# Kernel tuning notes

Measured on AMD Instinct MI355X. Metric: run time of the kernel, lower is better.

Reference implementation:

```python
import jax, jax.numpy as jnp
import numpy as np

H = 16        # num_attention_heads
D = 1024      # hidden_size
HD = D // H   # head_dim = 64


def setup_inputs() -> dict:
    key = jax.random.key(0)
    ks = jax.random.split(key, 5)
    B, T = 16, 1024
    s_in = 1.0 / np.sqrt(D)
    return {
        "hidden_states": jax.random.normal(ks[0], (B, T, D), dtype=jnp.float32),
        "w_qkv": jax.random.normal(ks[1], (D, 3 * D), dtype=jnp.float32) * s_in,
        "b_qkv": jnp.zeros((3 * D,), dtype=jnp.float32),
        "w_out": jax.random.normal(ks[2], (D, D), dtype=jnp.float32) * s_in,
        "b_out": jnp.zeros((D,), dtype=jnp.float32),
    }


def reference(hidden_states, w_qkv, b_qkv, w_out, b_out):
    B, T, C = hidden_states.shape
    qkv = hidden_states @ w_qkv + b_qkv                      # [B,T,3C]
    q, k, v = jnp.split(qkv, 3, axis=-1)
    # [B,T,C] -> [B,H,T,HD]
    q = q.reshape(B, T, H, HD).transpose(0, 2, 1, 3)
    k = k.reshape(B, T, H, HD).transpose(0, 2, 1, 3)
    v = v.reshape(B, T, H, HD).transpose(0, 2, 1, 3)
    scale = 1.0 / np.sqrt(HD)
    logits = jnp.einsum("bhqd,bhkd->bhqk", q, k) * scale     # [B,H,T,T]
    attn = jax.nn.softmax(logits, axis=-1)
    out = jnp.einsum("bhqk,bhkd->bhqd", attn, v)             # [B,H,T,HD]
    out = out.transpose(0, 2, 1, 3).reshape(B, T, C)
    return out @ w_out + b_out
```

## Files before the change

kernel.cpp:

```cpp
#include <hip/hip_runtime.h>
#include <cstdint>
#include <cstddef>

typedef _Float16 h8 __attribute__((ext_vector_type(8)));
typedef _Float16 h4 __attribute__((ext_vector_type(4)));
typedef float f4 __attribute__((ext_vector_type(4)));

#define MFMA(a, b, c) __builtin_amdgcn_mfma_f32_16x16x32_f16((a), (b), (c), 0, 0, 0)

__device__ __forceinline__ void gl_lds16(const void* g, void* l) {
  __builtin_amdgcn_global_load_lds((const __attribute__((address_space(1))) void*)g,
                                   (__attribute__((address_space(3))) void*)l, 16, 0, 0);
}

__global__ void k_cvt_hs(const float* __restrict__ in, _Float16* __restrict__ out, int n8) {
  int i = blockIdx.x * blockDim.x + threadIdx.x;
  if (i >= n8) return;
  size_t idx = (size_t)i * 8;
  float4 a = *(const float4*)(in + idx);
  float4 b = *(const float4*)(in + idx + 4);
  h8 o;
  o[0] = (_Float16)a.x; o[1] = (_Float16)a.y; o[2] = (_Float16)a.z; o[3] = (_Float16)a.w;
  o[4] = (_Float16)b.x; o[5] = (_Float16)b.y; o[6] = (_Float16)b.z; o[7] = (_Float16)b.w;
  *(h8*)(out + idx) = o;
}

__global__ void k_transcvt(const float* __restrict__ in, _Float16* __restrict__ out, int N, int K) {
  __shared__ float tile[64 * 65];
  int tn = blockIdx.x * 64, tk = blockIdx.y * 64;
  for (int i = 0; i < 4; ++i) {
    int cid = i * 256 + threadIdx.x;
    int r = cid >> 4, c4 = cid & 15;
    float4 v = *(const float4*)(in + (size_t)(tk + r) * N + tn + c4 * 4);
    tile[r * 65 + c4 * 4 + 0] = v.x; tile[r * 65 + c4 * 4 + 1] = v.y;
    tile[r * 65 + c4 * 4 + 2] = v.z; tile[r * 65 + c4 * 4 + 3] = v.w;
  }
  __syncthreads();
  for (int i = 0; i < 2; ++i) {
    int cid = i * 256 + threadIdx.x;
    int n = cid >> 3, kc = cid & 7;
    h8 o;
    for (int j = 0; j < 8; ++j) o[j] = (_Float16)tile[(kc * 8 + j) * 65 + n];
    *(h8*)(out + (size_t)(tn + n) * K + tk + kc * 8) = o;
  }
}

__global__ void k_transpose_v(const _Float16* __restrict__ V, _Float16* __restrict__ Vt) {
  __shared__ _Float16 tile[64 * 66];
  int bh = blockIdx.x;
  int tt = blockIdx.y * 64;
  const _Float16* src = V + (size_t)bh * 65536 + (size_t)tt * 64;
  _Float16* dst = Vt + (size_t)bh * 65536 + tt;
  for (int i = 0; i < 2; ++i) {
    int cid = i * 256 + threadIdx.x;
    int r = cid >> 3, c8 = cid & 7;
    h8 v = *(const h8*)(src + (size_t)r * 64 + c8 * 8);
    for (int j = 0; j < 8; ++j) tile[r * 66 + c8 * 8 + j] = v[j];
  }
  __syncthreads();
  for (int i = 0; i < 2; ++i) {
    int cid = i * 256 + threadIdx.x;
    int d = cid >> 3, tc = cid & 7;
    h8 o;
    for (int j = 0; j < 8; ++j) o[j] = tile[(tc * 8 + j) * 66 + d];
    *(h8*)(dst + (size_t)d * 1024 + tc * 8) = o;
  }
}

__global__ __launch_bounds__(256) void k_gemm_qkv(
    const _Float16* __restrict__ A, const _Float16* __restrict__ BT,
    const float* __restrict__ bias,
    _Float16* __restrict__ Q, _Float16* __restrict__ Kq, _Float16* __restrict__ V) {
  __shared__ _Float16 sA[128 * 64];
  __shared__ _Float16 sB[128 * 64];
  const int K = 1024;
  int tid = threadIdx.x, wave = tid >> 6, lane = tid & 63;
  int l15 = lane & 15, l4 = lane >> 4;
  int tm = blockIdx.y * 128, tn = blockIdx.x * 128;
  int wm = (wave & 1) * 64, wn = (wave >> 1) * 64;
  f4 acc[4][4] = {};
  for (int kt = 0; kt < K; kt += 64) {
    __syncthreads();
    for (int i = 0; i < 4; ++i) {
      int cid = i * 256 + tid;
      int r = cid >> 3, cs = cid & 7, cg = cs ^ (r & 7);
      gl_lds16(A + (size_t)(tm + r) * K + kt + cg * 8, (char*)sA + cid * 16);
      gl_lds16(BT + (size_t)(tn + r) * K + kt + cg * 8, (char*)sB + cid * 16);
    }
    __syncthreads();
    for (int k0 = 0; k0 < 64; k0 += 32) {
      h8 af[4], bf[4];
      int ch = (k0 >> 3) + l4;
      for (int mi = 0; mi < 4; ++mi) {
        int r = wm + mi * 16 + l15;
        af[mi] = *(const h8*)((const char*)sA + ((r * 8 + (ch ^ (r & 7))) * 16));
      }
      for (int ni = 0; ni < 4; ++ni) {
        int r = wn + ni * 16 + l15;
        bf[ni] = *(const h8*)((const char*)sB + ((r * 8 + (ch ^ (r & 7))) * 16));
      }
      for (int mi = 0; mi < 4; ++mi)
        for (int ni = 0; ni < 4; ++ni)
          acc[mi][ni] = MFMA(af[mi], bf[ni], acc[mi][ni]);
    }
  }
  for (int mi = 0; mi < 4; ++mi) {
    for (int ni = 0; ni < 4; ++ni) {
      int n = tn + wn + ni * 16 + l15;
      float bv = bias[n];
      int which = n >> 10, h = (n >> 6) & 15, d = n & 63;
      _Float16* dst = which == 0 ? Q : (which == 1 ? Kq : V);
      for (int r = 0; r < 4; ++r) {
        int m = tm + wm + mi * 16 + l4 * 4 + r;
        int b = m >> 10, t = m & 1023;
        dst[(((size_t)b * 16 + h) * 1024 + t) * 64 + d] = (_Float16)(acc[mi][ni][r] + bv);
      }
    }
  }
}

__global__ __launch_bounds__(256, 4) void k_attn(
    const _Float16* __restrict__ Q, const _Float16* __restrict__ Kk,
    const _Float16* __restrict__ Vt, _Float16* __restrict__ O) {
  __shared__ char smem[18432 + 8192 + 8192];
  _Float16* sQ = (_Float16*)smem;
  _Float16* sP = (_Float16*)smem;
  _Float16* sK = (_Float16*)(smem + 18432);
  _Float16* sV = (_Float16*)(smem + 18432 + 8192);
  const float SCL = 0.125f * 1.44269504088896340736f;
  int tid = threadIdx.x, wave = tid >> 6, lane = tid & 63;
  int l15 = lane & 15, l4 = lane >> 4;
  int bh = blockIdx.y;
  int qt = blockIdx.x * 128;
  const _Float16* Qb = Q + (size_t)bh * 65536;
  const _Float16* Kb = Kk + (size_t)bh * 65536;
  const _Float16* Vb = Vt + (size_t)bh * 65536;

  for (int i = 0; i < 4; ++i) {
    int cid = i * 256 + tid;
    int r = cid >> 3, cs = cid & 7, cg = cs ^ (r & 7);
    gl_lds16(Qb + (size_t)(qt + r) * 64 + cg * 8, (char*)sQ + cid * 16);
  }
  __syncthreads();
  h8 qf[2][2];
  for (int nt = 0; nt < 2; ++nt) {
    int r = wave * 32 + nt * 16 + l15;
    for (int kk = 0; kk < 2; ++kk) {
      int ch = kk * 4 + l4;
      qf[nt][kk] = *(const h8*)((const char*)sQ + ((r * 8 + (ch ^ (r & 7))) * 16));
    }
  }
  _Float16 scl_h = (_Float16)SCL;
  for (int nt = 0; nt < 2; ++nt)
    for (int kk = 0; kk < 2; ++kk)
      for (int j = 0; j < 8; ++j) qf[nt][kk][j] *= scl_h;

  float lpart[2] = {0.f, 0.f};
  f4 oacc[2][4] = {};
  _Float16* pw = sP + wave * 32 * 72;

  for (int kt = 0; kt < 1024; kt += 64) {
    __syncthreads();
    for (int i = 0; i < 2; ++i) {
      int cid = i * 256 + tid;
      int r = cid >> 3, cs = cid & 7, cg = cs ^ (r & 7);
      gl_lds16(Kb + (size_t)(kt + r) * 64 + cg * 8, (char*)sK + cid * 16);
      gl_lds16(Vb + (size_t)r * 1024 + kt + cg * 8, (char*)sV + cid * 16);
    }
    __syncthreads();
    f4 sacc[4][2] = {};
    for (int kk = 0; kk < 2; ++kk) {
      h8 kf[4];
      int ch = kk * 4 + l4;
      for (int mt = 0; mt < 4; ++mt) {
        int r = mt * 16 + l15;
        kf[mt] = *(const h8*)((const char*)sK + ((r * 8 + (ch ^ (r & 7))) * 16));
      }
      for (int mt = 0; mt < 4; ++mt)
        for (int nt = 0; nt < 2; ++nt)
          sacc[mt][nt] = MFMA(kf[mt], qf[nt][kk], sacc[mt][nt]);
    }
    for (int mt = 0; mt < 4; ++mt) {
      for (int nt = 0; nt < 2; ++nt) {
        float p0 = exp2f(sacc[mt][nt][0]);
        float p1 = exp2f(sacc[mt][nt][1]);
        float p2 = exp2f(sacc[mt][nt][2]);
        float p3 = exp2f(sacc[mt][nt][3]);
        lpart[nt] += (p0 + p1) + (p2 + p3);
        h4 pk;
        pk[0] = (_Float16)p0; pk[1] = (_Float16)p1;
        pk[2] = (_Float16)p2; pk[3] = (_Float16)p3;
        *(h4*)(pw + (nt * 16 + l15) * 72 + mt * 16 + l4 * 4) = pk;
      }
    }
    for (int kk = 0; kk < 2; ++kk) {
      h8 pf[2], vf[4];
      for (int mi = 0; mi < 2; ++mi)
        pf[mi] = *(const h8*)(pw + (mi * 16 + l15) * 72 + kk * 32 + l4 * 8);
      int ch = kk * 4 + l4;
      for (int nd = 0; nd < 4; ++nd) {
        int r = nd * 16 + l15;
        vf[nd] = *(const h8*)((const char*)sV + ((r * 8 + (ch ^ (r & 7))) * 16));
      }
      for (int mi = 0; mi < 2; ++mi)
        for (int nd = 0; nd < 4; ++nd)
          oacc[mi][nd] = MFMA(pf[mi], vf[nd], oacc[mi][nd]);
    }
  }
  float lt[2];
  lt[0] = lpart[0]; lt[1] = lpart[1];
  for (int nt = 0; nt < 2; ++nt) {
    lt[nt] += __shfl_xor(lt[nt], 16);
    lt[nt] += __shfl_xor(lt[nt], 32);
  }
  int b = bh >> 4, h = bh & 15;
  for (int mi = 0; mi < 2; ++mi) {
    for (int r = 0; r < 4; ++r) {
      float lr = __shfl(lt[mi], l4 * 4 + r);
      float inv = 1.f / lr;
      int t = qt + wave * 32 + mi * 16 + l4 * 4 + r;
      for (int nd = 0; nd < 4; ++nd)
        O[(size_t)(b * 1024 + t) * 1024 + h * 64 + nd * 16 + l15] =
            (_Float16)(oacc[mi][nd][r] * inv);
    }
  }
}

__global__ __launch_bounds__(256) void k_gemm_out(
    const _Float16* __restrict__ A, const _Float16* __restrict__ BT,
    const float* __restrict__ bias, float* __restrict__ C) {
  __shared__ _Float16 sA[128 * 64];
  __shared__ _Float16 sB[128 * 64];
  const int K = 1024;
  int tid = threadIdx.x, wave = tid >> 6, lane = tid & 63;
  int l15 = lane & 15, l4 = lane >> 4;
  int tm = blockIdx.y * 128, tn = blockIdx.x * 128;
  int wm = (wave & 1) * 64, wn = (wave >> 1) * 64;
  f4 acc[4][4] = {};
  for (int kt = 0; kt < K; kt += 64) {
    __syncthreads();
    for (int i = 0; i < 4; ++i) {
      int cid = i * 256 + tid;
      int r = cid >> 3, cs = cid & 7, cg = cs ^ (r & 7);
      gl_lds16(A + (size_t)(tm + r) * K + kt + cg * 8, (char*)sA + cid * 16);
      gl_lds16(BT + (size_t)(tn + r) * K + kt + cg * 8, (char*)sB + cid * 16);
    }
    __syncthreads();
    for (int k0 = 0; k0 < 64; k0 += 32) {
      h8 af[4], bf[4];
      int ch = (k0 >> 3) + l4;
      for (int mi = 0; mi < 4; ++mi) {
        int r = wm + mi * 16 + l15;
        af[mi] = *(const h8*)((const char*)sA + ((r * 8 + (ch ^ (r & 7))) * 16));
      }
      for (int ni = 0; ni < 4; ++ni) {
        int r = wn + ni * 16 + l15;
        bf[ni] = *(const h8*)((const char*)sB + ((r * 8 + (ch ^ (r & 7))) * 16));
      }
      for (int mi = 0; mi < 4; ++mi)
        for (int ni = 0; ni < 4; ++ni)
          acc[mi][ni] = MFMA(af[mi], bf[ni], acc[mi][ni]);
    }
  }
  for (int mi = 0; mi < 4; ++mi) {
    for (int ni = 0; ni < 4; ++ni) {
      int n = tn + wn + ni * 16 + l15;
      float bv = bias[n];
      for (int r = 0; r < 4; ++r) {
        int m = tm + wm + mi * 16 + l4 * 4 + r;
        C[(size_t)m * 1024 + n] = acc[mi][ni][r] + bv;
      }
    }
  }
}

extern "C" void kernel_launch(void* const* d_in, const int* in_sizes, int n_in,
                              void* d_out, int out_size, void* d_ws, size_t ws_size,
                              hipStream_t stream) {
  const float* hs    = (const float*)d_in[0];
  const float* w_qkv = (const float*)d_in[1];
  const float* b_qkv = (const float*)d_in[2];
  const float* w_out = (const float*)d_in[3];
  const float* b_out = (const float*)d_in[4];
  float* out = (float*)d_out;
  char* ws = (char*)d_ws;

  _Float16* hs_h  = (_Float16*)(ws);
  _Float16* wqkvT = (_Float16*)(ws + 33554432);
  _Float16* woutT = (_Float16*)(ws + 39845888);
  _Float16* q_ws  = (_Float16*)(ws + 41943040);
  _Float16* k_ws  = (_Float16*)(ws + 75497472);
  _Float16* v_ws  = (_Float16*)(ws + 109051904);
  _Float16* vt_ws = (_Float16*)(ws + 142606336);

  k_cvt_hs<<<8192, 256, 0, stream>>>(hs, hs_h, 2097152);
  k_transcvt<<<dim3(48, 16), 256, 0, stream>>>(w_qkv, wqkvT, 3072, 1024);
  k_transcvt<<<dim3(16, 16), 256, 0, stream>>>(w_out, woutT, 1024, 1024);
  k_gemm_qkv<<<dim3(24, 128), 256, 0, stream>>>(hs_h, wqkvT, b_qkv, q_ws, k_ws, v_ws);
  k_transpose_v<<<dim3(256, 16), 256, 0, stream>>>(v_ws, vt_ws);
  _Float16* attn_h = hs_h;
  k_attn<<<dim3(8, 256), 256, 0, stream>>>(q_ws, k_ws, vt_ws, attn_h);
  k_gemm_out<<<dim3(8, 128), 256, 0, stream>>>(attn_h, woutT, b_out, out);
}
```

Measured before the change: 435.7 us.

## Fuse V transpose into QKV GEMM epilogue and enlarge attention query tile

The QKV GEMM epilogue now writes V directly in transposed [b,h,d,t] layout by staging the tile in shared memory, which removes the separate transpose kernel and its extra pass over V in global memory. The attention kernel now processes 256 queries per block (64 per wave) instead of 128, so each K/V tile loaded into LDS is reused across twice as many queries. In exchange the attention kernel uses more registers and LDS, and launch bounds drop to 3 blocks per CU, which lowers occupancy.

```diff
diff --git a/kernel.cpp b/kernel.cpp
--- a/kernel.cpp
+++ b/kernel.cpp
@@ -45,34 +45,13 @@
   }
 }
 
-__global__ void k_transpose_v(const _Float16* __restrict__ V, _Float16* __restrict__ Vt) {
-  __shared__ _Float16 tile[64 * 66];
-  int bh = blockIdx.x;
-  int tt = blockIdx.y * 64;
-  const _Float16* src = V + (size_t)bh * 65536 + (size_t)tt * 64;
-  _Float16* dst = Vt + (size_t)bh * 65536 + tt;
-  for (int i = 0; i < 2; ++i) {
-    int cid = i * 256 + threadIdx.x;
-    int r = cid >> 3, c8 = cid & 7;
-    h8 v = *(const h8*)(src + (size_t)r * 64 + c8 * 8);
-    for (int j = 0; j < 8; ++j) tile[r * 66 + c8 * 8 + j] = v[j];
-  }
-  __syncthreads();
-  for (int i = 0; i < 2; ++i) {
-    int cid = i * 256 + threadIdx.x;
-    int d = cid >> 3, tc = cid & 7;
-    h8 o;
-    for (int j = 0; j < 8; ++j) o[j] = tile[(tc * 8 + j) * 66 + d];
-    *(h8*)(dst + (size_t)d * 1024 + tc * 8) = o;
-  }
-}
-
 __global__ __launch_bounds__(256) void k_gemm_qkv(
     const _Float16* __restrict__ A, const _Float16* __restrict__ BT,
     const float* __restrict__ bias,
-    _Float16* __restrict__ Q, _Float16* __restrict__ Kq, _Float16* __restrict__ V) {
-  __shared__ _Float16 sA[128 * 64];
-  __shared__ _Float16 sB[128 * 64];
+    _Float16* __restrict__ Q, _Float16* __restrict__ Kq, _Float16* __restrict__ Vt) {
+  __shared__ char smem[32768];
+  _Float16* sA = (_Float16*)smem;
+  _Float16* sB = (_Float16*)(smem + 16384);
   const int K = 1024;
   int tid = threadIdx.x, wave = tid >> 6, lane = tid & 63;
   int l15 = lane & 15, l4 = lane >> 4;
@@ -104,60 +83,91 @@
           acc[mi][ni] = MFMA(af[mi], bf[ni], acc[mi][ni]);
     }
   }
-  for (int mi = 0; mi < 4; ++mi) {
-    for (int ni = 0; ni < 4; ++ni) {
-      int n = tn + wn + ni * 16 + l15;
-      float bv = bias[n];
-      int which = n >> 10, h = (n >> 6) & 15, d = n & 63;
-      _Float16* dst = which == 0 ? Q : (which == 1 ? Kq : V);
-      for (int r = 0; r < 4; ++r) {
-        int m = tm + wm + mi * 16 + l4 * 4 + r;
-        int b = m >> 10, t = m & 1023;
-        dst[(((size_t)b * 16 + h) * 1024 + t) * 64 + d] = (_Float16)(acc[mi][ni][r] + bv);
-      }
-    }
-  }
-}
-
-__global__ __launch_bounds__(256, 4) void k_attn(
+  if (blockIdx.x < 16) {
+    for (int mi = 0; mi < 4; ++mi) {
+      for (int ni = 0; ni < 4; ++ni) {
+        int n = tn + wn + ni * 16 + l15;
+        float bv = bias[n];
+        int which = n >> 10, h = (n >> 6) & 15, d = n & 63;
+        _Float16* dst = which == 0 ? Q : Kq;
+        for (int r = 0; r < 4; ++r) {
+          int m = tm + wm + mi * 16 + l4 * 4 + r;
+          int b = m >> 10, t = m & 1023;
+          dst[(((size_t)b * 16 + h) * 1024 + t) * 64 + d] = (_Float16)(acc[mi][ni][r] + bv);
+        }
+      }
+    }
+  } else {
+    _Float16* L = (_Float16*)smem;
+    int b = tm >> 10, tbase = tm & 1023;
+    for (int pass = 0; pass < 2; ++pass) {
+      __syncthreads();
+      if ((wave & 1) == pass) {
+        for (int mi = 0; mi < 4; ++mi) {
+          int t_local = mi * 16 + l4 * 4;
+          for (int ni = 0; ni < 4; ++ni) {
+            int n_local = wn + ni * 16 + l15;
+            float bv = bias[tn + n_local];
+            h4 pk;
+            for (int r = 0; r < 4; ++r) pk[r] = (_Float16)(acc[mi][ni][r] + bv);
+            *(h4*)(L + n_local * 68 + t_local) = pk;
+          }
+        }
+      }
+      __syncthreads();
+      for (int it = 0; it < 2; ++it) {
+        int n_local = it * 64 + (tid >> 2);
+        int h = (tn - 2048 + n_local) >> 6;
+        int d = n_local & 63;
+        size_t row = (((size_t)b * 16 + h) * 64 + d) * 1024 + tbase + pass * 64;
+        for (int j = 0; j < 2; ++j) {
+          int th = (tid & 3) * 8 + j * 32;
+          *(h8*)(Vt + row + th) = *(const h8*)(L + n_local * 68 + th);
+        }
+      }
+    }
+  }
+}
+
+__global__ __launch_bounds__(256, 3) void k_attn(
     const _Float16* __restrict__ Q, const _Float16* __restrict__ Kk,
     const _Float16* __restrict__ Vt, _Float16* __restrict__ O) {
-  __shared__ char smem[18432 + 8192 + 8192];
+  __shared__ char smem[36864 + 8192 + 8192];
   _Float16* sQ = (_Float16*)smem;
   _Float16* sP = (_Float16*)smem;
-  _Float16* sK = (_Float16*)(smem + 18432);
-  _Float16* sV = (_Float16*)(smem + 18432 + 8192);
+  _Float16* sK = (_Float16*)(smem + 36864);
+  _Float16* sV = (_Float16*)(smem + 36864 + 8192);
   const float SCL = 0.125f * 1.44269504088896340736f;
   int tid = threadIdx.x, wave = tid >> 6, lane = tid & 63;
   int l15 = lane & 15, l4 = lane >> 4;
   int bh = blockIdx.y;
-  int qt = blockIdx.x * 128;
+  int qt = blockIdx.x * 256;
   const _Float16* Qb = Q + (size_t)bh * 65536;
   const _Float16* Kb = Kk + (size_t)bh * 65536;
   const _Float16* Vb = Vt + (size_t)bh * 65536;
 
-  for (int i = 0; i < 4; ++i) {
+  for (int i = 0; i < 8; ++i) {
     int cid = i * 256 + tid;
     int r = cid >> 3, cs = cid & 7, cg = cs ^ (r & 7);
     gl_lds16(Qb + (size_t)(qt + r) * 64 + cg * 8, (char*)sQ + cid * 16);
   }
   __syncthreads();
-  h8 qf[2][2];
-  for (int nt = 0; nt < 2; ++nt) {
-    int r = wave * 32 + nt * 16 + l15;
+  h8 qf[4][2];
+  for (int nt = 0; nt < 4; ++nt) {
+    int r = wave * 64 + nt * 16 + l15;
     for (int kk = 0; kk < 2; ++kk) {
       int ch = kk * 4 + l4;
       qf[nt][kk] = *(const h8*)((const char*)sQ + ((r * 8 + (ch ^ (r & 7))) * 16));
     }
   }
   _Float16 scl_h = (_Float16)SCL;
-  for (int nt = 0; nt < 2; ++nt)
+  for (int nt = 0; nt < 4; ++nt)
     for (int kk = 0; kk < 2; ++kk)
       for (int j = 0; j < 8; ++j) qf[nt][kk][j] *= scl_h;
 
-  float lpart[2] = {0.f, 0.f};
-  f4 oacc[2][4] = {};
-  _Float16* pw = sP + wave * 32 * 72;
+  float lpart[4] = {0.f, 0.f, 0.f, 0.f};
+  f4 oacc[4][4] = {};
+  _Float16* pw = sP + wave * 64 * 72;
 
   for (int kt = 0; kt < 1024; kt += 64) {
     __syncthreads();
@@ -168,57 +178,59 @@
       gl_lds16(Vb + (size_t)r * 1024 + kt + cg * 8, (char*)sV + cid * 16);
     }
     __syncthreads();
-    f4 sacc[4][2] = {};
+    for (int mh = 0; mh < 2; ++mh) {
+      f4 sacc[2][4] = {};
+      for (int kk = 0; kk < 2; ++kk) {
+        h8 kf[2];
+        int ch = kk * 4 + l4;
+        for (int mt = 0; mt < 2; ++mt) {
+          int r = mh * 32 + mt * 16 + l15;
+          kf[mt] = *(const h8*)((const char*)sK + ((r * 8 + (ch ^ (r & 7))) * 16));
+        }
+        for (int mt = 0; mt < 2; ++mt)
+          for (int nt = 0; nt < 4; ++nt)
+            sacc[mt][nt] = MFMA(kf[mt], qf[nt][kk], sacc[mt][nt]);
+      }
+      for (int mt = 0; mt < 2; ++mt) {
+        for (int nt = 0; nt < 4; ++nt) {
+          float p0 = exp2f(sacc[mt][nt][0]);
+          float p1 = exp2f(sacc[mt][nt][1]);
+          float p2 = exp2f(sacc[mt][nt][2]);
+          float p3 = exp2f(sacc[mt][nt][3]);
+          lpart[nt] += (p0 + p1) + (p2 + p3);
+          h4 pk;
+          pk[0] = (_Float16)p0; pk[1] = (_Float16)p1;
+          pk[2] = (_Float16)p2; pk[3] = (_Float16)p3;
+          *(h4*)(pw + (nt * 16 + l15) * 72 + mh * 32 + mt * 16 + l4 * 4) = pk;
+        }
+      }
+    }
     for (int kk = 0; kk < 2; ++kk) {
-      h8 kf[4];
-      int ch = kk * 4 + l4;
-      for (int mt = 0; mt < 4; ++mt) {
-        int r = mt * 16 + l15;
-        kf[mt] = *(const h8*)((const char*)sK + ((r * 8 + (ch ^ (r & 7))) * 16));
-      }
-      for (int mt = 0; mt < 4; ++mt)
-        for (int nt = 0; nt < 2; ++nt)
-          sacc[mt][nt] = MFMA(kf[mt], qf[nt][kk], sacc[mt][nt]);
-    }
-    for (int mt = 0; mt < 4; ++mt) {
-      for (int nt = 0; nt < 2; ++nt) {
-        float p0 = exp2f(sacc[mt][nt][0]);
-        float p1 = exp2f(sacc[mt][nt][1]);
-        float p2 = exp2f(sacc[mt][nt][2]);
-        float p3 = exp2f(sacc[mt][nt][3]);
-        lpart[nt] += (p0 + p1) + (p2 + p3);
-        h4 pk;
-        pk[0] = (_Float16)p0; pk[1] = (_Float16)p1;
-        pk[2] = (_Float16)p2; pk[3] = (_Float16)p3;
-        *(h4*)(pw + (nt * 16 + l15) * 72 + mt * 16 + l4 * 4) = pk;
-      }
-    }
-    for (int kk = 0; kk < 2; ++kk) {
-      h8 pf[2], vf[4];
-      for (int mi = 0; mi < 2; ++mi)
+      h8 pf[4], vf[4];
+      for (int mi = 0; mi < 4; ++mi)
         pf[mi] = *(const h8*)(pw + (mi * 16 + l15) * 72 + kk * 32 + l4 * 8);
       int ch = kk * 4 + l4;
       for (int nd = 0; nd < 4; ++nd) {
         int r = nd * 16 + l15;
         vf[nd] = *(const h8*)((const char*)sV + ((r * 8 + (ch ^ (r & 7))) * 16));
       }
-      for (int mi = 0; mi < 2; ++mi)
+      for (int mi = 0; mi < 4; ++mi)
         for (int nd = 0; nd < 4; ++nd)
           oacc[mi][nd] = MFMA(pf[mi], vf[nd], oacc[mi][nd]);
     }
   }
-  float lt[2];
-  lt[0] = lpart[0]; lt[1] = lpart[1];
-  for (int nt = 0; nt < 2; ++nt) {
+  float lt[4];
+  for (int nt = 0; nt < 4; ++nt) {
+    lt[nt] = lpart[nt];
     lt[nt] += __shfl_xor(lt[nt], 16);
     lt[nt] += __shfl_xor(lt[nt], 32);
   }
   int b = bh >> 4, h = bh & 15;
-  for (int mi = 0; mi < 2; ++mi) {
+  for (int mi = 0; mi < 4; ++mi) {
     for (int r = 0; r < 4; ++r) {
       float lr = __shfl(lt[mi], l4 * 4 + r);
       float inv = 1.f / lr;
-      int t = qt + wave * 32 + mi * 16 + l4 * 4 + r;
+      int t = qt + wave * 64 + mi * 16 + l4 * 4 + r;
       for (int nd = 0; nd < 4; ++nd)
         O[(size_t)(b * 1024 + t) * 1024 + h * 64 + nd * 16 + l15] =
             (_Float16)(oacc[mi][nd][r] * inv);
@@ -290,15 +302,13 @@
   _Float16* woutT = (_Float16*)(ws + 39845888);
   _Float16* q_ws  = (_Float16*)(ws + 41943040);
   _Float16* k_ws  = (_Float16*)(ws + 75497472);
-  _Float16* v_ws  = (_Float16*)(ws + 109051904);
-  _Float16* vt_ws = (_Float16*)(ws + 142606336);
+  _Float16* vt_ws = (_Float16*)(ws + 109051904);
 
   k_cvt_hs<<<8192, 256, 0, stream>>>(hs, hs_h, 2097152);
   k_transcvt<<<dim3(48, 16), 256, 0, stream>>>(w_qkv, wqkvT, 3072, 1024);
   k_transcvt<<<dim3(16, 16), 256, 0, stream>>>(w_out, woutT, 1024, 1024);
-  k_gemm_qkv<<<dim3(24, 128), 256, 0, stream>>>(hs_h, wqkvT, b_qkv, q_ws, k_ws, v_ws);
-  k_transpose_v<<<dim3(256, 16), 256, 0, stream>>>(v_ws, vt_ws);
+  k_gemm_qkv<<<dim3(24, 128), 256, 0, stream>>>(hs_h, wqkvT, b_qkv, q_ws, k_ws, vt_ws);
   _Float16* attn_h = hs_h;
-  k_attn<<<dim3(8, 256), 256, 0, stream>>>(q_ws, k_ws, vt_ws, attn_h);
+  k_attn<<<dim3(4, 256), 256, 0, stream>>>(q_ws, k_ws, vt_ws, attn_h);
   k_gemm_out<<<dim3(8, 128), 256, 0, stream>>>(attn_h, woutT, b_out, out);
 }
```

Result: slower. 583.2 us (+33.9%).
